# Optimization experiments

Hardware: AMD Instinct MI355X
Metric: run time of the kernel (lower is better)

## Reference

```python
import jax, jax.numpy as jnp
import numpy as np

B, S, D, H, DFF, K = 16, 1024, 1024, 16, 4096, 3


def setup_inputs() -> dict:
    key = jax.random.key(0)
    ks = jax.random.split(key, 8)
    f = lambda k, sh: jax.random.normal(k, sh, jnp.float32) * 0.02
    return dict(
        x=jax.random.normal(ks[0], (B, S, D), jnp.float32),
        mask=jnp.ones((B, 1, S), jnp.int32),
        alpha1=jnp.ones((D,), jnp.float32), bias1=jnp.zeros((D,), jnp.float32),
        alpha2=jnp.ones((D,), jnp.float32), bias2=jnp.zeros((D,), jnp.float32),
        W_l1=f(ks[1], (D, 2 * D)), b_l1=jnp.zeros((2 * D,), jnp.float32),
        conv_w=f(ks[2], (H, K)),
        W_l2=f(ks[3], (D, D)), b_l2=jnp.zeros((D,), jnp.float32),
        W_ff1=f(ks[4], (D, DFF)), b_ff1=jnp.zeros((DFF,), jnp.float32),
        W_ff2=f(ks[5], (DFF, D)), b_ff2=jnp.zeros((D,), jnp.float32),
    )


def _norm(x, alpha, bias, eps=1e-6):
    # Norm: alpha * (x - mean) / (std + eps) + bias, torch std is unbiased (ddof=1)
    mu = x.mean(-1, keepdims=True)
    sd = x.std(-1, keepdims=True, ddof=1)
    return alpha * (x - mu) / (sd + eps) + bias


def _lightconv(x, conv_w):
    # x: [B, S, C]; conv_w: [H, K] softmax-normalized over K; channels in a head share kernel
    C = x.shape[-1]
    w = jax.nn.softmax(conv_w, axis=-1)              # [H, K]
    wk = jnp.repeat(w, C // H, axis=0)[:, None, :]   # [C, 1, K] depthwise kernel
    y = jax.lax.conv_general_dilated(
        x.transpose(0, 2, 1), wk, (1,), [(K // 2, (K - 1) // 2)],
        dimension_numbers=('NCH', 'OIH', 'NCH'), feature_group_count=C)
    return y.transpose(0, 2, 1)


def reference(x, mask, alpha1, bias1, alpha2, bias2, W_l1, b_l1, conv_w,
              W_l2, b_l2, W_ff1, b_ff1, W_ff2, b_ff2):
    # --- lightweight-conv sublayer ---
    res = x
    h = _norm(x, alpha1, bias1)
    h = h @ W_l1 + b_l1                         # [B,S,2C]
    a, b = jnp.split(h, 2, axis=-1)
    h = a * jax.nn.sigmoid(b)                   # GLU -> [B,S,C]
    cm = mask[:, -1, :][:, :, None]             # [B,S,1]
    h = jnp.where(cm == 0, 0.0, h)
    h = _lightconv(h, conv_w)
    h = h @ W_l2 + b_l2
    x = res + h
    # --- FFN sublayer ---
    res = x
    h = _norm(x, alpha2, bias2)
    h = jax.nn.relu(h @ W_ff1 + b_ff1) @ W_ff2 + b_ff2
    return res + h
```

## Files before the change

### kernel.cpp

```cpp
#include <hip/hip_runtime.h>

typedef unsigned short ushort_t;
typedef __attribute__((ext_vector_type(8))) short s8v;
typedef __attribute__((ext_vector_type(4))) float f4v;

__device__ __forceinline__ float b2f(ushort_t h) {
    union { unsigned u; float f; } c; c.u = ((unsigned)h) << 16; return c.f;
}
__device__ __forceinline__ ushort_t f2b(float f) {
    union { float f; unsigned u; } c; c.f = f;
    unsigned u = c.u;
    return (ushort_t)((u + 0x7fffu + ((u >> 16) & 1u)) >> 16);
}

__device__ __forceinline__ void glds16(const void* g, void* l) {
    __builtin_amdgcn_global_load_lds(
        (const __attribute__((address_space(1))) void*)g,
        (__attribute__((address_space(3))) void*)l, 16, 0, 0);
}

__global__ __launch_bounds__(256) void trans_k(const float* __restrict__ W,
                                               ushort_t* __restrict__ Wt,
                                               int K, int N) {
    __shared__ float tile[64][65];
    int k0 = blockIdx.x * 64, n0 = blockIdx.y * 64;
    int t = threadIdx.x;
    int c = t & 63, r4 = t >> 6;
#pragma unroll
    for (int i = 0; i < 16; ++i) {
        int r = i * 4 + r4;
        tile[r][c] = W[(size_t)(k0 + r) * N + n0 + c];
    }
    __syncthreads();
#pragma unroll
    for (int i = 0; i < 16; ++i) {
        int r = i * 4 + r4;
        Wt[(size_t)(n0 + r) * K + k0 + c] = f2b(tile[c][r]);
    }
}

__global__ __launch_bounds__(256) void norm_k(const float* __restrict__ x,
                                              const float* __restrict__ al,
                                              const float* __restrict__ be,
                                              ushort_t* __restrict__ out) {
    int row = blockIdx.x;
    const float4* xr = (const float4*)(x + (size_t)row * 1024);
    float4 v = xr[threadIdx.x];
    float s = v.x + v.y + v.z + v.w;
    float q = v.x * v.x + v.y * v.y + v.z * v.z + v.w * v.w;
#pragma unroll
    for (int o = 32; o > 0; o >>= 1) {
        s += __shfl_down(s, o);
        q += __shfl_down(q, o);
    }
    __shared__ float ss[4], qq[4];
    int lane = threadIdx.x & 63, wv = threadIdx.x >> 6;
    if (lane == 0) { ss[wv] = s; qq[wv] = q; }
    __syncthreads();
    s = ss[0] + ss[1] + ss[2] + ss[3];
    q = qq[0] + qq[1] + qq[2] + qq[3];
    float mu = s * (1.f / 1024.f);
    float var = (q - 1024.f * mu * mu) * (1.f / 1023.f);
    var = fmaxf(var, 0.f);
    float inv = 1.f / (sqrtf(var) + 1e-6f);
    float4 a4 = ((const float4*)al)[threadIdx.x];
    float4 b4 = ((const float4*)be)[threadIdx.x];
    ushort4 o4;
    o4.x = f2b(a4.x * (v.x - mu) * inv + b4.x);
    o4.y = f2b(a4.y * (v.y - mu) * inv + b4.y);
    o4.z = f2b(a4.z * (v.z - mu) * inv + b4.z);
    o4.w = f2b(a4.w * (v.w - mu) * inv + b4.w);
    ((ushort4*)(out + (size_t)row * 1024))[threadIdx.x] = o4;
}

__global__ __launch_bounds__(256) void gluconv_k(const ushort_t* __restrict__ t1,
                                                 const int* __restrict__ mask,
                                                 const float* __restrict__ cw,
                                                 ushort_t* __restrict__ out) {
    int i = blockIdx.x * 256 + threadIdx.x;
    int row = i >> 7;
    int cc = (i & 127) << 3;
    int b = row >> 10, s = row & 1023;
    int head = cc >> 6;
    float w0 = cw[head * 3 + 0], w1 = cw[head * 3 + 1], w2 = cw[head * 3 + 2];
    float mx = fmaxf(w0, fmaxf(w1, w2));
    float e0 = __expf(w0 - mx), e1 = __expf(w1 - mx), e2 = __expf(w2 - mx);
    float inv = 1.f / (e0 + e1 + e2);
    float wt[3] = {e0 * inv, e1 * inv, e2 * inv};
    float a8[8] = {0.f, 0.f, 0.f, 0.f, 0.f, 0.f, 0.f, 0.f};
#pragma unroll
    for (int tap = 0; tap < 3; ++tap) {
        int ss = s + tap - 1;
        if (ss < 0 || ss > 1023) continue;
        float wm = (mask[b * 1024 + ss] == 0) ? 0.f : wt[tap];
        size_t base = (size_t)(row + tap - 1) * 2048 + cc;
        s8v va = *(const s8v*)(t1 + base);
        s8v vb = *(const s8v*)(t1 + base + 1024);
#pragma unroll
        for (int j = 0; j < 8; ++j) {
            float a = b2f((ushort_t)va[j]);
            float xx = b2f((ushort_t)vb[j]);
            float sg = 1.f / (1.f + __expf(-xx));
            a8[j] += wm * a * sg;
        }
    }
    s8v ov;
#pragma unroll
    for (int j = 0; j < 8; ++j) ov[j] = (short)f2b(a8[j]);
    *(s8v*)(out + (size_t)row * 1024 + cc) = ov;
}

template <int EPI>
__global__ __launch_bounds__(512, 4) void gemm_k(const ushort_t* __restrict__ A,
                                                 const ushort_t* __restrict__ Bt,
                                                 const float* __restrict__ bias,
                                                 const float* res, float* outf,
                                                 ushort_t* outb, int N, int K) {
    __shared__ char smem[73728] __attribute__((aligned(128)));
    const int NBN = N >> 8;
    const int nwg = gridDim.x;
    const int per = nwg >> 3;
    const int tt = (blockIdx.x & 7) * per + (blockIdx.x >> 3);
    const int gw = NBN << 4;
    const int g = tt / gw;
    const int rem = tt - g * gw;
    const int bm = (g << 4) + (rem & 15);
    const int bn = rem >> 4;

    const int t = threadIdx.x;
    const int l = t & 63, w = t >> 6;
    const int wm = w >> 2, wn = w & 3;
    const int lr = l & 15, lk = l >> 4;

    const int swzel = (((t & 3) ^ ((t >> 3) & 3)) << 3);
    const int r0 = t >> 2;
    const ushort_t* pA0 = A + (size_t)(bm * 128 + r0) * K + swzel;
    const ushort_t* pB0 = Bt + (size_t)(bn * 256 + r0) * K + swzel;
    const ushort_t* pB1 = pB0 + (size_t)128 * K;

    const int fswz = ((lk ^ ((lr >> 1) & 3)) << 4);
    int aoff[4], boff[4];
#pragma unroll
    for (int m = 0; m < 4; ++m)
        aoff[m] = (wm * 64 + m * 16 + lr) * 64 + fswz;
#pragma unroll
    for (int n = 0; n < 4; ++n)
        boff[n] = 8192 + (wn * 64 + n * 16 + lr) * 64 + fswz;

    f4v acc[4][4];
#pragma unroll
    for (int m = 0; m < 4; ++m)
#pragma unroll
        for (int n = 0; n < 4; ++n) acc[m][n] = f4v{0.f, 0.f, 0.f, 0.f};

    const int NK = K >> 5;

    {
        char* d0 = smem + t * 16;
        glds16(pA0 + 0, d0);
        glds16(pB0 + 0, d0 + 8192);
        glds16(pB1 + 0, d0 + 16384);
        char* d1 = smem + 24576 + t * 16;
        glds16(pA0 + 32, d1);
        glds16(pB0 + 32, d1 + 8192);
        glds16(pB1 + 32, d1 + 16384);
    }
    asm volatile("s_waitcnt vmcnt(3)");
    __builtin_amdgcn_s_barrier();
    __builtin_amdgcn_sched_barrier(0);

    int cur = 0;
    for (int i = 0; i < NK; ++i) {
        const char* cb = smem + cur;
        int nx2 = cur + 49152; if (nx2 >= 73728) nx2 -= 73728;
        int st = i + 2; if (st >= NK) st = NK - 1;
        const int ko = st * 32;
        char* sd = smem + nx2 + t * 16;

        glds16(pA0 + ko, sd);
        glds16(pB0 + ko, sd + 8192);
        glds16(pB1 + ko, sd + 16384);

        s8v aF[4], bF[4];
#pragma unroll
        for (int m = 0; m < 4; ++m) aF[m] = *(const s8v*)(cb + aoff[m]);
#pragma unroll
        for (int n = 0; n < 4; ++n) bF[n] = *(const s8v*)(cb + boff[n]);
        __builtin_amdgcn_s_setprio(1);
#pragma unroll
        for (int m = 0; m < 4; ++m)
#pragma unroll
            for (int n = 0; n < 4; ++n)
                acc[m][n] = __builtin_amdgcn_mfma_f32_16x16x32_bf16(
                    aF[m], bF[n], acc[m][n], 0, 0, 0);
        __builtin_amdgcn_s_setprio(0);

        __builtin_amdgcn_sched_barrier(0);
        asm volatile("s_waitcnt lgkmcnt(0)");
        asm volatile("s_waitcnt vmcnt(3)");
        __builtin_amdgcn_s_barrier();
        __builtin_amdgcn_sched_barrier(0);

        cur += 24576; if (cur >= 73728) cur = 0;
    }

    asm volatile("s_waitcnt vmcnt(0)");
    __builtin_amdgcn_s_barrier();

    if (EPI == 1) {
#pragma unroll
        for (int n = 0; n < 4; ++n) {
            int gcol = bn * 256 + wn * 64 + n * 16 + lr;
            float bb = bias[gcol];
#pragma unroll
            for (int m = 0; m < 4; ++m) {
#pragma unroll
                for (int r = 0; r < 4; ++r) {
                    int grow = bm * 128 + wm * 64 + m * 16 + lk * 4 + r;
                    size_t oi = (size_t)grow * N + gcol;
                    outf[oi] = acc[m][n][r] + bb + res[oi];
                }
            }
        }
    } else {
        float bb4[4];
#pragma unroll
        for (int n = 0; n < 4; ++n)
            bb4[n] = bias[bn * 256 + wn * 64 + n * 16 + lr];
#pragma unroll
        for (int m = 0; m < 4; ++m)
#pragma unroll
            for (int n = 0; n < 4; ++n)
#pragma unroll
                for (int r = 0; r < 4; ++r) {
                    int row = wm * 64 + m * 16 + lk * 4 + r;
                    int colb = ((wn * 64 + n * 16 + lr) * 2) ^ ((row & 3) << 4);
                    float v = acc[m][n][r] + bb4[n];
                    if (EPI == 2) v = fmaxf(v, 0.f);
                    *(ushort_t*)(smem + row * 512 + colb) = f2b(v);
                }
        __builtin_amdgcn_s_barrier();
#pragma unroll
        for (int s = 0; s < 8; ++s) {
            int row = s * 16 + (t >> 5);
            int byt = row * 512 + (((t & 31) * 16) ^ ((row & 3) << 4));
            int grow = bm * 128 + row;
            int gcol = bn * 256 + (t & 31) * 8;
            *(s8v*)(outb + (size_t)grow * N + gcol) = *(const s8v*)(smem + byt);
        }
    }
}

extern "C" void kernel_launch(void* const* d_in, const int* in_sizes, int n_in,
                              void* d_out, int out_size, void* d_ws, size_t ws_size,
                              hipStream_t stream) {
    const float* x      = (const float*)d_in[0];
    const int*   mask   = (const int*)d_in[1];
    const float* alpha1 = (const float*)d_in[2];
    const float* bias1  = (const float*)d_in[3];
    const float* alpha2 = (const float*)d_in[4];
    const float* bias2  = (const float*)d_in[5];
    const float* W_l1   = (const float*)d_in[6];
    const float* b_l1   = (const float*)d_in[7];
    const float* conv_w = (const float*)d_in[8];
    const float* W_l2   = (const float*)d_in[9];
    const float* b_l2   = (const float*)d_in[10];
    const float* W_ff1  = (const float*)d_in[11];
    const float* b_ff1  = (const float*)d_in[12];
    const float* W_ff2  = (const float*)d_in[13];
    const float* b_ff2  = (const float*)d_in[14];
    float* out = (float*)d_out;

    char* ws = (char*)d_ws;
    size_t off = 0;
    auto alloc = [&](size_t b) {
        char* p = ws + off;
        off += (b + 255) & ~(size_t)255;
        return p;
    };
    ushort_t* Wl1t  = (ushort_t*)alloc(2048ull * 1024 * 2);
    ushort_t* Wl2t  = (ushort_t*)alloc(1024ull * 1024 * 2);
    ushort_t* Wff1t = (ushort_t*)alloc(4096ull * 1024 * 2);
    ushort_t* Wff2t = (ushort_t*)alloc(1024ull * 4096 * 2);
    char* regA = alloc(134217728ull);
    ushort_t* B1 = (ushort_t*)alloc(33554432ull);
    ushort_t* C1 = (ushort_t*)alloc(33554432ull);
    ushort_t* t1 = (ushort_t*)regA;
    ushort_t* f1 = (ushort_t*)regA;

    const int R = 16384;

    trans_k<<<dim3(16, 32), 256, 0, stream>>>(W_l1, Wl1t, 1024, 2048);
    trans_k<<<dim3(16, 16), 256, 0, stream>>>(W_l2, Wl2t, 1024, 1024);
    trans_k<<<dim3(16, 64), 256, 0, stream>>>(W_ff1, Wff1t, 1024, 4096);
    trans_k<<<dim3(64, 16), 256, 0, stream>>>(W_ff2, Wff2t, 4096, 1024);

    norm_k<<<R, 256, 0, stream>>>(x, alpha1, bias1, B1);
    gemm_k<0><<<128 * 8, 512, 0, stream>>>(B1, Wl1t, b_l1, nullptr, nullptr, t1, 2048, 1024);
    gluconv_k<<<8192, 256, 0, stream>>>(t1, mask, conv_w, C1);
    gemm_k<1><<<128 * 4, 512, 0, stream>>>(C1, Wl2t, b_l2, x, out, nullptr, 1024, 1024);

    norm_k<<<R, 256, 0, stream>>>(out, alpha2, bias2, B1);
    gemm_k<2><<<128 * 16, 512, 0, stream>>>(B1, Wff1t, b_ff1, nullptr, nullptr, f1, 4096, 1024);
    gemm_k<1><<<128 * 4, 512, 0, stream>>>(f1, Wff2t, b_ff2, out, out, nullptr, 1024, 4096);
}
```

Before: 613.1 us.

## Fuse GLU and mask into first GEMM epilogue; shrink GEMM tiles to 128x128

```diff
diff --git a/kernel.cpp b/kernel.cpp
--- a/kernel.cpp
+++ b/kernel.cpp
@@ -19,6 +19,7 @@
         (__attribute__((address_space(3))) void*)l, 16, 0, 0);
 }
 
+template <int PERM>
 __global__ __launch_bounds__(256) void trans_k(const float* __restrict__ W,
                                                ushort_t* __restrict__ Wt,
                                                int K, int N) {
@@ -35,7 +36,16 @@
 #pragma unroll
     for (int i = 0; i < 16; ++i) {
         int r = i * 4 + r4;
-        Wt[(size_t)(n0 + r) * K + k0 + c] = f2b(tile[c][r]);
+        int s = n0 + r;
+        int d;
+        if (PERM) {
+            int a = (s < 1024);
+            int s2 = a ? s : s - 1024;
+            d = ((s2 >> 6) << 7) + (a ? 0 : 64) + (s2 & 63);
+        } else {
+            d = s;
+        }
+        Wt[(size_t)d * K + k0 + c] = f2b(tile[c][r]);
     }
 }
 
@@ -73,70 +83,61 @@
     ((ushort4*)(out + (size_t)row * 1024))[threadIdx.x] = o4;
 }
 
-__global__ __launch_bounds__(256) void gluconv_k(const ushort_t* __restrict__ t1,
-                                                 const int* __restrict__ mask,
-                                                 const float* __restrict__ cw,
-                                                 ushort_t* __restrict__ out) {
+__global__ __launch_bounds__(256) void conv_k(const ushort_t* __restrict__ g,
+                                              const float* __restrict__ cw,
+                                              ushort_t* __restrict__ out) {
     int i = blockIdx.x * 256 + threadIdx.x;
     int row = i >> 7;
     int cc = (i & 127) << 3;
-    int b = row >> 10, s = row & 1023;
+    int s = row & 1023;
     int head = cc >> 6;
     float w0 = cw[head * 3 + 0], w1 = cw[head * 3 + 1], w2 = cw[head * 3 + 2];
     float mx = fmaxf(w0, fmaxf(w1, w2));
     float e0 = __expf(w0 - mx), e1 = __expf(w1 - mx), e2 = __expf(w2 - mx);
     float inv = 1.f / (e0 + e1 + e2);
-    float wt[3] = {e0 * inv, e1 * inv, e2 * inv};
-    float a8[8] = {0.f, 0.f, 0.f, 0.f, 0.f, 0.f, 0.f, 0.f};
-#pragma unroll
-    for (int tap = 0; tap < 3; ++tap) {
-        int ss = s + tap - 1;
-        if (ss < 0 || ss > 1023) continue;
-        float wm = (mask[b * 1024 + ss] == 0) ? 0.f : wt[tap];
-        size_t base = (size_t)(row + tap - 1) * 2048 + cc;
-        s8v va = *(const s8v*)(t1 + base);
-        s8v vb = *(const s8v*)(t1 + base + 1024);
-#pragma unroll
-        for (int j = 0; j < 8; ++j) {
-            float a = b2f((ushort_t)va[j]);
-            float xx = b2f((ushort_t)vb[j]);
-            float sg = 1.f / (1.f + __expf(-xx));
-            a8[j] += wm * a * sg;
-        }
-    }
+    w0 = e0 * inv; w1 = e1 * inv; w2 = e2 * inv;
+    size_t base = (size_t)row * 1024 + cc;
+    s8v z = {0, 0, 0, 0, 0, 0, 0, 0};
+    s8v vm = (s > 0)    ? *(const s8v*)(g + base - 1024) : z;
+    s8v v0 = *(const s8v*)(g + base);
+    s8v vp = (s < 1023) ? *(const s8v*)(g + base + 1024) : z;
     s8v ov;
 #pragma unroll
-    for (int j = 0; j < 8; ++j) ov[j] = (short)f2b(a8[j]);
-    *(s8v*)(out + (size_t)row * 1024 + cc) = ov;
+    for (int j = 0; j < 8; ++j) {
+        float r = w0 * b2f((ushort_t)vm[j]) + w1 * b2f((ushort_t)v0[j]) +
+                  w2 * b2f((ushort_t)vp[j]);
+        ov[j] = (short)f2b(r);
+    }
+    *(s8v*)(out + base) = ov;
 }
 
 template <int EPI>
-__global__ __launch_bounds__(512, 4) void gemm_k(const ushort_t* __restrict__ A,
+__global__ __launch_bounds__(256, 4) void gemm_k(const ushort_t* __restrict__ A,
                                                  const ushort_t* __restrict__ Bt,
                                                  const float* __restrict__ bias,
+                                                 const int* __restrict__ maskp,
                                                  const float* res, float* outf,
                                                  ushort_t* outb, int N, int K) {
-    __shared__ char smem[73728] __attribute__((aligned(128)));
-    const int NBN = N >> 8;
-    const int nwg = gridDim.x;
-    const int per = nwg >> 3;
+    __shared__ char smem[32768] __attribute__((aligned(128)));
+    const int NBN = N >> 7;
+    const int per = gridDim.x >> 3;
     const int tt = (blockIdx.x & 7) * per + (blockIdx.x >> 3);
-    const int gw = NBN << 4;
+    const int gw = NBN << 3;
     const int g = tt / gw;
     const int rem = tt - g * gw;
-    const int bm = (g << 4) + (rem & 15);
-    const int bn = rem >> 4;
+    const int bm = (g << 3) + (rem & 7);
+    const int bn = rem >> 3;
 
     const int t = threadIdx.x;
     const int l = t & 63, w = t >> 6;
-    const int wm = w >> 2, wn = w & 3;
+    const int wm = w >> 1, wn = w & 1;
     const int lr = l & 15, lk = l >> 4;
 
     const int swzel = (((t & 3) ^ ((t >> 3) & 3)) << 3);
-    const int r0 = t >> 2;
-    const ushort_t* pA0 = A + (size_t)(bm * 128 + r0) * K + swzel;
-    const ushort_t* pB0 = Bt + (size_t)(bn * 256 + r0) * K + swzel;
-    const ushort_t* pB1 = pB0 + (size_t)128 * K;
+    const ushort_t* pA0 = A + (size_t)(bm * 128 + (t >> 2)) * K + swzel;
+    const ushort_t* pA1 = pA0 + (size_t)64 * K;
+    const ushort_t* pB0 = Bt + (size_t)(bn * 128 + (t >> 2)) * K + swzel;
+    const ushort_t* pB1 = pB0 + (size_t)64 * K;
 
     const int fswz = ((lk ^ ((lr >> 1) & 3)) << 4);
     int aoff[4], boff[4];
@@ -155,31 +156,24 @@
 
     const int NK = K >> 5;
 
-    {
-        char* d0 = smem + t * 16;
-        glds16(pA0 + 0, d0);
-        glds16(pB0 + 0, d0 + 8192);
-        glds16(pB1 + 0, d0 + 16384);
-        char* d1 = smem + 24576 + t * 16;
-        glds16(pA0 + 32, d1);
-        glds16(pB0 + 32, d1 + 8192);
-        glds16(pB1 + 32, d1 + 16384);
-    }
-    asm volatile("s_waitcnt vmcnt(3)");
+    glds16(pA0, smem + t * 16);
+    glds16(pA1, smem + 4096 + t * 16);
+    glds16(pB0, smem + 8192 + t * 16);
+    glds16(pB1, smem + 12288 + t * 16);
+    asm volatile("s_waitcnt vmcnt(0)");
     __builtin_amdgcn_s_barrier();
     __builtin_amdgcn_sched_barrier(0);
 
-    int cur = 0;
     for (int i = 0; i < NK; ++i) {
-        const char* cb = smem + cur;
-        int nx2 = cur + 49152; if (nx2 >= 73728) nx2 -= 73728;
-        int st = i + 2; if (st >= NK) st = NK - 1;
+        const char* cb = smem + (size_t)(i & 1) * 16384;
+        int st = (i + 1 < NK) ? i + 1 : NK - 1;
         const int ko = st * 32;
-        char* sd = smem + nx2 + t * 16;
+        char* sd = smem + (size_t)((i + 1) & 1) * 16384 + t * 16;
 
         glds16(pA0 + ko, sd);
+        glds16(pA1 + ko, sd + 4096);
         glds16(pB0 + ko, sd + 8192);
-        glds16(pB1 + ko, sd + 16384);
+        glds16(pB1 + ko, sd + 12288);
 
         s8v aF[4], bF[4];
 #pragma unroll
@@ -196,21 +190,15 @@
         __builtin_amdgcn_s_setprio(0);
 
         __builtin_amdgcn_sched_barrier(0);
-        asm volatile("s_waitcnt lgkmcnt(0)");
-        asm volatile("s_waitcnt vmcnt(3)");
+        asm volatile("s_waitcnt vmcnt(0)");
         __builtin_amdgcn_s_barrier();
         __builtin_amdgcn_sched_barrier(0);
-
-        cur += 24576; if (cur >= 73728) cur = 0;
-    }
-
-    asm volatile("s_waitcnt vmcnt(0)");
-    __builtin_amdgcn_s_barrier();
+    }
 
     if (EPI == 1) {
 #pragma unroll
         for (int n = 0; n < 4; ++n) {
-            int gcol = bn * 256 + wn * 64 + n * 16 + lr;
+            int gcol = bn * 128 + wn * 64 + n * 16 + lr;
             float bb = bias[gcol];
 #pragma unroll
             for (int m = 0; m < 4; ++m) {
@@ -223,10 +211,16 @@
             }
         }
     } else {
+        __builtin_amdgcn_s_barrier();
         float bb4[4];
 #pragma unroll
-        for (int n = 0; n < 4; ++n)
-            bb4[n] = bias[bn * 256 + wn * 64 + n * 16 + lr];
+        for (int n = 0; n < 4; ++n) {
+            int d = bn * 128 + wn * 64 + n * 16 + lr;
+            int src = d;
+            if (EPI == 3)
+                src = (((d >> 6) & 1) << 10) + ((d >> 7) << 6) + (d & 63);
+            bb4[n] = bias[src];
+        }
 #pragma unroll
         for (int m = 0; m < 4; ++m)
 #pragma unroll
@@ -237,16 +231,38 @@
                     int colb = ((wn * 64 + n * 16 + lr) * 2) ^ ((row & 3) << 4);
                     float v = acc[m][n][r] + bb4[n];
                     if (EPI == 2) v = fmaxf(v, 0.f);
-                    *(ushort_t*)(smem + row * 512 + colb) = f2b(v);
+                    *(ushort_t*)(smem + row * 256 + colb) = f2b(v);
                 }
         __builtin_amdgcn_s_barrier();
-#pragma unroll
-        for (int s = 0; s < 8; ++s) {
-            int row = s * 16 + (t >> 5);
-            int byt = row * 512 + (((t & 31) * 16) ^ ((row & 3) << 4));
-            int grow = bm * 128 + row;
-            int gcol = bn * 256 + (t & 31) * 8;
-            *(s8v*)(outb + (size_t)grow * N + gcol) = *(const s8v*)(smem + byt);
+        if (EPI == 3) {
+#pragma unroll
+            for (int s = 0; s < 4; ++s) {
+                int row = s * 32 + (t >> 3);
+                int j = t & 7;
+                int abyt = row * 256 + ((j * 16) ^ ((row & 3) << 4));
+                s8v av = *(const s8v*)(smem + abyt);
+                s8v bv = *(const s8v*)(smem + abyt + 128);
+                int grow = bm * 128 + row;
+                float mval = (maskp[grow] == 0) ? 0.f : 1.f;
+                s8v ov;
+#pragma unroll
+                for (int jj = 0; jj < 8; ++jj) {
+                    float a = b2f((ushort_t)av[jj]);
+                    float xx = b2f((ushort_t)bv[jj]);
+                    ov[jj] = (short)f2b(a * mval / (1.f + __expf(-xx)));
+                }
+                *(s8v*)(outb + (size_t)grow * (N >> 1) + bn * 64 + j * 8) = ov;
+            }
+        } else {
+#pragma unroll
+            for (int s = 0; s < 8; ++s) {
+                int row = s * 16 + (t >> 4);
+                int byt = row * 256 + (((t & 15) * 16) ^ ((row & 3) << 4));
+                int grow = bm * 128 + row;
+                int gcol = bn * 128 + (t & 15) * 8;
+                *(s8v*)(outb + (size_t)grow * N + gcol) =
+                    *(const s8v*)(smem + byt);
+            }
         }
     }
 }
@@ -285,22 +301,26 @@
     char* regA = alloc(134217728ull);
     ushort_t* B1 = (ushort_t*)alloc(33554432ull);
     ushort_t* C1 = (ushort_t*)alloc(33554432ull);
-    ushort_t* t1 = (ushort_t*)regA;
+    ushort_t* G1 = (ushort_t*)regA;
     ushort_t* f1 = (ushort_t*)regA;
 
     const int R = 16384;
 
-    trans_k<<<dim3(16, 32), 256, 0, stream>>>(W_l1, Wl1t, 1024, 2048);
-    trans_k<<<dim3(16, 16), 256, 0, stream>>>(W_l2, Wl2t, 1024, 1024);
-    trans_k<<<dim3(16, 64), 256, 0, stream>>>(W_ff1, Wff1t, 1024, 4096);
-    trans_k<<<dim3(64, 16), 256, 0, stream>>>(W_ff2, Wff2t, 4096, 1024);
+    trans_k<1><<<dim3(16, 32), 256, 0, stream>>>(W_l1, Wl1t, 1024, 2048);
+    trans_k<0><<<dim3(16, 16), 256, 0, stream>>>(W_l2, Wl2t, 1024, 1024);
+    trans_k<0><<<dim3(16, 64), 256, 0, stream>>>(W_ff1, Wff1t, 1024, 4096);
+    trans_k<0><<<dim3(64, 16), 256, 0, stream>>>(W_ff2, Wff2t, 4096, 1024);
 
     norm_k<<<R, 256, 0, stream>>>(x, alpha1, bias1, B1);
-    gemm_k<0><<<128 * 8, 512, 0, stream>>>(B1, Wl1t, b_l1, nullptr, nullptr, t1, 2048, 1024);
-    gluconv_k<<<8192, 256, 0, stream>>>(t1, mask, conv_w, C1);
-    gemm_k<1><<<128 * 4, 512, 0, stream>>>(C1, Wl2t, b_l2, x, out, nullptr, 1024, 1024);
+    gemm_k<3><<<128 * 16, 256, 0, stream>>>(B1, Wl1t, b_l1, mask, nullptr,
+                                            nullptr, G1, 2048, 1024);
+    conv_k<<<8192, 256, 0, stream>>>(G1, conv_w, C1);
+    gemm_k<1><<<128 * 8, 256, 0, stream>>>(C1, Wl2t, b_l2, nullptr, x, out,
+                                           nullptr, 1024, 1024);
 
     norm_k<<<R, 256, 0, stream>>>(out, alpha2, bias2, B1);
-    gemm_k<2><<<128 * 16, 512, 0, stream>>>(B1, Wff1t, b_ff1, nullptr, nullptr, f1, 4096, 1024);
-    gemm_k<1><<<128 * 4, 512, 0, stream>>>(f1, Wff2t, b_ff2, out, out, nullptr, 1024, 4096);
-}
+    gemm_k<2><<<128 * 32, 256, 0, stream>>>(B1, Wff1t, b_ff1, nullptr, nullptr,
+                                            nullptr, f1, 4096, 1024);
+    gemm_k<1><<<128 * 8, 256, 0, stream>>>(f1, Wff2t, b_ff2, nullptr, out, out,
+                                           nullptr, 1024, 4096);
+}
```

Result: faster. 591.3 us (-3.6%).
